# Optimization experiments

Measured on AMD Instinct MI355X. Metric: run time of the kernel, lower is better.

## Reference

```python
import jax, jax.numpy as jnp
from jax import lax
import numpy as np

DN = ('NCHW', 'OIHW', 'NCHW')

def conv2d(x, w, b, pad):
    y = lax.conv_general_dilated(x, w, (1, 1), [(pad, pad), (pad, pad)], dimension_numbers=DN)
    return y + b[None, :, None, None]

def setup_inputs() -> dict:
    key = jax.random.key(0)
    ks = jax.random.split(key, 20)
    B, C, H, W = 2, 256, 64, 64
    d = {}
    d['Fl'] = jax.random.normal(ks[0], (B, C, H, W), dtype=jnp.float32)
    d['Fv'] = jax.random.normal(ks[1], (B, C, H, W), dtype=jnp.float32)
    s3 = 1.0 / np.sqrt(C * 9)
    s1 = 1.0 / np.sqrt(C)
    names3 = ['Wqs', 'Wks', 'Wvs', 'Wqc', 'Wkc', 'Wvc']
    for i, n in enumerate(names3):
        d[n] = jax.random.normal(ks[2 + 2 * i], (C, C, 3, 3), dtype=jnp.float32) * s3
        d['b' + n[1:]] = jax.random.normal(ks[3 + 2 * i], (C,), dtype=jnp.float32) * 0.01
    d['Wgs'] = jax.random.normal(ks[14], (C, C, 1, 1), dtype=jnp.float32) * s1
    d['bgs'] = jax.random.normal(ks[15], (C,), dtype=jnp.float32) * 0.01
    d['Wfuse'] = jax.random.normal(ks[16], (C, 2 * C, 1, 1), dtype=jnp.float32) * (1.0 / np.sqrt(2 * C))
    d['bfuse'] = jax.random.normal(ks[17], (C,), dtype=jnp.float32) * 0.01
    return d

def reference(Fl, Fv, Wqs, bqs, Wks, bks, Wvs, bvs, Wqc, bqc, Wkc, bkc, Wvc, bvc, Wgs, bgs, Wfuse, bfuse):
    b, c, h, w = Fl.shape
    hw = h * w
    # --- self branch (on Fl) ---
    Qs = conv2d(Fl, Wqs, bqs, 1).reshape(b, c, hw)
    Ks = conv2d(Fl, Wks, bks, 1).reshape(b, c, hw)
    Vs = conv2d(Fl, Wvs, bvs, 1).reshape(b, c, hw)
    multi_s = jnp.einsum('bjk,bjq->bkq', Qs, Ks)          # [b, hw, hw]
    multi_s = jax.nn.softmax(multi_s, axis=1)              # softmax over dim=1 (as in torch code)
    Gs = jnp.einsum('bik,bjk->bij', multi_s, Vs)           # [b, hw, c]
    Gs = Gs.reshape(b, c, h, w)                            # raw reshape, faithful to torch
    Gs = conv2d(Gs, Wgs, bgs, 0) + Fl
    # --- cross branch (Q from Fl, K/V from Fv) ---
    Qc = conv2d(Fl, Wqc, bqc, 1).reshape(b, c, hw)
    Kc = conv2d(Fv, Wkc, bkc, 1).reshape(b, c, hw)
    Vc = conv2d(Fv, Wvc, bvc, 1).reshape(b, c, hw)
    multi_c = jnp.einsum('bjk,bjq->bkq', Qc, Kc)
    multi_c = jax.nn.softmax(multi_c, axis=1)
    Gc = jnp.einsum('bik,bjk->bij', multi_c, Vc)
    Gc = Gc.reshape(b, c, h, w)
    Gc = conv2d(Gc, Wgs, bgs, 0) + Fv                      # note: original uses Gs_conv for both branches
    out = conv2d(jnp.concatenate([Gs, Gc], axis=1), Wfuse, bfuse, 0)
    return out
```

## Files before the change

kernel.cpp:

```cpp
#include <hip/hip_runtime.h>

typedef __bf16 bf16x4 __attribute__((ext_vector_type(4)));
typedef __bf16 bf16x8 __attribute__((ext_vector_type(8)));
typedef float  f32x4  __attribute__((ext_vector_type(4)));

#define HWSZ 4096
#define CCH  256
#define LOG2E 1.44269504088896340736f

enum { M_SSTAT = 0, M_CONV = 1, M_G1 = 4, M_FUSE = 5 };

__device__ __forceinline__ float exp2_fast(float x) {
#if __has_builtin(__builtin_amdgcn_exp2f)
  return __builtin_amdgcn_exp2f(x);
#else
  return exp2f(x);
#endif
}

__device__ __forceinline__ void stage16(const __bf16* g, __bf16* ldsBase) {
#if __has_builtin(__builtin_amdgcn_global_load_lds)
  __builtin_amdgcn_global_load_lds(
      (const __attribute__((address_space(1))) void*)g,
      (__attribute__((address_space(3))) void*)ldsBase, 16, 0, 0);
#else
  int lane = threadIdx.x & 63;
  *(bf16x8*)(ldsBase + lane * 8) = *(const bf16x8*)g;
#endif
}

template<int MODE>
__global__ __launch_bounds__(256)
void gemm_bt(const __bf16* __restrict__ A, long sAz,
             const __bf16* __restrict__ B, long sBz,
             int N, int K,
             __bf16* __restrict__ o0, __bf16* __restrict__ o1,
             __bf16* __restrict__ o2, __bf16* __restrict__ o3,
             long sOz,
             float* __restrict__ fout, long sFz,
             const float* __restrict__ bb0, const float* __restrict__ bb1,
             const float* __restrict__ bb2, const float* __restrict__ bb3,
             const float* __restrict__ resid, long sRz,
             float* __restrict__ pmo, float* __restrict__ plo,
             __bf16* __restrict__ o4, __bf16* __restrict__ o5,
             const float* __restrict__ bb4, const float* __restrict__ bb5,
             const __bf16* __restrict__ A2)
{
  __shared__ __align__(16) __bf16 smem[8192];
  __bf16* As = smem;
  __bf16* Bs = smem + 4096;

  const int tid  = threadIdx.x;
  const int lane = tid & 63;
  const int w    = tid >> 6;
  const int wm   = (w >> 1) * 64;
  const int wn   = (w & 1) * 64;
  const int z    = blockIdx.z;
  const int by   = blockIdx.y;
  const int bn   = blockIdx.x * 128;

  int bmEff = by * 128;
  const __bf16* Ab;
  const __bf16* Bb;
  if constexpr (MODE == M_CONV) {
    bool isL = (by < 8);
    bmEff = (isL ? by : by - 8) * 128;
    Ab = isL ? A : A2;
    Bb = B + (long)((isL ? 0 : 2) + z) * sBz;
  } else {
    Ab = A + (long)z * sAz;
    Bb = B + (long)z * sBz;
  }

  f32x4 acc[4][4] = {};

  const int srow = lane >> 2;
  const int skc  = (lane & 3) * 8;

  for (int k0 = 0; k0 < K; k0 += 32) {
#pragma unroll
    for (int j = 0; j < 2; ++j) {
      int rbase = w * 32 + j * 16;
      stage16(Ab + (long)(bmEff + rbase + srow) * K + k0 + skc, As + rbase * 32);
    }
#pragma unroll
    for (int j = 0; j < 2; ++j) {
      int rbase = w * 32 + j * 16;
      stage16(Bb + (long)(bn + rbase + srow) * K + k0 + skc, Bs + rbase * 32);
    }
    __syncthreads();
    bf16x8 af[4], bfr[4];
#pragma unroll
    for (int t = 0; t < 4; ++t)
      af[t] = *(const bf16x8*)(As + (wm + t * 16 + (lane & 15)) * 32 + (lane >> 4) * 8);
#pragma unroll
    for (int t = 0; t < 4; ++t)
      bfr[t] = *(const bf16x8*)(Bs + (wn + t * 16 + (lane & 15)) * 32 + (lane >> 4) * 8);
#pragma unroll
    for (int mt = 0; mt < 4; ++mt)
#pragma unroll
      for (int nt = 0; nt < 4; ++nt)
        acc[mt][nt] = __builtin_amdgcn_mfma_f32_16x16x32_bf16(af[mt], bfr[nt], acc[mt][nt], 0, 0, 0);
    __syncthreads();
  }

  if constexpr (MODE != M_SSTAT) {
#pragma unroll
    for (int mt = 0; mt < 4; ++mt) {
#pragma unroll
      for (int nt = 0; nt < 4; ++nt) {
#pragma unroll
        for (int r = 0; r < 4; ++r) {
          int m = bmEff + wm + mt * 16 + (lane >> 4) * 4 + r;
          int n = bn + wn + nt * 16 + (lane & 15);
          float v = acc[mt][nt][r];
          if constexpr (MODE == M_CONV) {
            int g = m >> 8, mm = m & 255;
            const float* bias; __bf16* op; bool vlay;
            if (by < 8) {
              bias = (g == 0) ? bb0 : (g == 1) ? bb1 : (g == 2) ? bb2 : bb3;
              op   = (g == 0) ? o0  : (g == 1) ? o1  : (g == 2) ? o2  : o3;
              vlay = (g == 2);
            } else {
              bias = g ? bb5 : bb4;
              op   = g ? o5  : o4;
              vlay = (g == 1);
            }
            float vv = v + bias[mm];
            if (vlay) op[(long)z * sOz + (long)mm * HWSZ + n] = (__bf16)vv;
            else      op[(long)z * sOz + (long)n * CCH + mm] = (__bf16)vv;
          } else if constexpr (MODE == M_G1) {
            int bz = z & 1, brr = z >> 1;
            const float* rs = brr ? bb4 : resid;
            float vv = v + bb0[m] + rs[(long)bz * sRz + (long)m * HWSZ + n];
            o0[(long)bz * sOz + (long)n * 512 + m + brr * 256] = (__bf16)vv;
          } else if constexpr (MODE == M_FUSE) {
            fout[(long)z * sFz + (long)m * HWSZ + n] = v + bb0[m];
          }
        }
      }
    }
  }

  if constexpr (MODE == M_SSTAT) {
    __shared__ float sm_[4][64], sl_[4][64];
#pragma unroll
    for (int nt = 0; nt < 4; ++nt) {
      float mx = -3.0e38f;
#pragma unroll
      for (int mt = 0; mt < 4; ++mt)
#pragma unroll
        for (int r = 0; r < 4; ++r) mx = fmaxf(mx, acc[mt][nt][r]);
      float sl = 0.f;
#pragma unroll
      for (int mt = 0; mt < 4; ++mt)
#pragma unroll
        for (int r = 0; r < 4; ++r) sl += exp2_fast((acc[mt][nt][r] - mx) * LOG2E);
#pragma unroll
      for (int d = 16; d <= 32; d <<= 1) {
        float om = __shfl_xor(mx, d, 64);
        float ol = __shfl_xor(sl, d, 64);
        float nm = fmaxf(mx, om);
        sl = sl * exp2_fast((mx - nm) * LOG2E) + ol * exp2_fast((om - nm) * LOG2E);
        mx = nm;
      }
      if (lane < 16) { sm_[w][nt * 16 + lane] = mx; sl_[w][nt * 16 + lane] = sl; }
    }
    __syncthreads();
    if (tid < 128) {
      int hf = tid >> 6, c = tid & 63;
      float m1 = sm_[hf][c],     l1 = sl_[hf][c];
      float m2 = sm_[hf + 2][c], l2 = sl_[hf + 2][c];
      float nm = fmaxf(m1, m2);
      float ll = l1 * exp2_fast((m1 - nm) * LOG2E) + l2 * exp2_fast((m2 - nm) * LOG2E);
      pmo[((long)z * 32 + by) * 4096 + bn + tid] = nm;
      plo[((long)z * 32 + by) * 4096 + bn + tid] = ll;
    }
  }
}

__global__ __launch_bounds__(256)
void fused_pv(const __bf16* __restrict__ qs, const __bf16* __restrict__ qc,
              const __bf16* __restrict__ ks, const __bf16* __restrict__ kc,
              const __bf16* __restrict__ vs, const __bf16* __restrict__ vc,
              const float* __restrict__ mst, const float* __restrict__ lst,
              float* __restrict__ gacc)
{
  __shared__ __align__(16) __bf16 Qres[64 * 260];
  __shared__ __align__(16) __bf16 Pl[64 * 132];
  __shared__ __align__(16) __bf16 Kst[128 * 32];
  __shared__ __align__(16) __bf16 Vst[256 * 32];
  __shared__ float ms_[128], li_[128];

  const int tid = threadIdx.x, lane = tid & 63, w = tid >> 6;
  const int quad = lane >> 4, l15 = lane & 15;
  const int bi  = blockIdx.x * 64;
  const int zbr = blockIdx.y;
  const int qh  = blockIdx.z;
  const int br = zbr >> 1, z = zbr & 1;
  const __bf16* Qt = (br ? qc : qs) + (long)z * 1048576;
  const __bf16* Kt = (br ? kc : ks) + (long)z * 1048576;
  const __bf16* Vv = (br ? vc : vs) + (long)z * 1048576;
  const float* msp = mst + (long)zbr * 4096;
  const float* lsp = lst + (long)zbr * 4096;
  float* go = gacc + ((long)qh * 4 + zbr) * 1048576;

  for (int idx = tid; idx < 2048; idx += 256) {
    int r = idx >> 5, c8 = (idx & 31) * 8;
    *(bf16x8*)(Qres + r * 260 + c8) = *(const bf16x8*)(Qt + (long)(bi + r) * 256 + c8);
  }

  f32x4 accO[4][4] = {};
  const int srow = lane >> 2, skc = (lane & 3) * 8;
  const int q0 = qh * 2048;

  for (int qc0 = q0; qc0 < q0 + 2048; qc0 += 128) {
    if (tid < 128) ms_[tid] = msp[qc0 + tid];
    else           li_[tid - 128] = lsp[qc0 + tid - 128];
    f32x4 accS[4][2] = {};
#pragma unroll
    for (int cs = 0; cs < 256; cs += 32) {
#pragma unroll
      for (int jj = 0; jj < 2; ++jj) {
        int rbase = w * 32 + jj * 16;
        stage16(Kt + (long)(qc0 + rbase + srow) * 256 + cs + skc, Kst + rbase * 32);
      }
      __syncthreads();
      bf16x8 aq[4], bk[2];
#pragma unroll
      for (int mt = 0; mt < 4; ++mt)
        aq[mt] = *(const bf16x8*)(Qres + (mt * 16 + l15) * 260 + cs + quad * 8);
#pragma unroll
      for (int nt = 0; nt < 2; ++nt)
        bk[nt] = *(const bf16x8*)(Kst + (w * 32 + nt * 16 + l15) * 32 + quad * 8);
#pragma unroll
      for (int mt = 0; mt < 4; ++mt)
#pragma unroll
        for (int nt = 0; nt < 2; ++nt)
          accS[mt][nt] = __builtin_amdgcn_mfma_f32_16x16x32_bf16(aq[mt], bk[nt], accS[mt][nt], 0, 0, 0);
      __syncthreads();
    }
#pragma unroll
    for (int mt = 0; mt < 4; ++mt)
#pragma unroll
      for (int nt = 0; nt < 2; ++nt) {
        int q = w * 32 + nt * 16 + l15;
        float mq = ms_[q], lq = li_[q];
#pragma unroll
        for (int r = 0; r < 4; ++r) {
          int i = mt * 16 + quad * 4 + r;
          Pl[i * 132 + q] = (__bf16)(exp2_fast((accS[mt][nt][r] - mq) * LOG2E) * lq);
        }
      }
    __syncthreads();
#pragma unroll
    for (int qs0 = 0; qs0 < 128; qs0 += 32) {
#pragma unroll
      for (int c = 0; c < 4; ++c) {
        int rbase = w * 64 + c * 16;
        stage16(Vv + (long)(rbase + srow) * 4096 + qc0 + qs0 + skc, Vst + rbase * 32);
      }
      __syncthreads();
      bf16x8 ap[4], bv[4];
#pragma unroll
      for (int mt = 0; mt < 4; ++mt)
        ap[mt] = *(const bf16x8*)(Pl + (mt * 16 + l15) * 132 + qs0 + quad * 8);
#pragma unroll
      for (int nt = 0; nt < 4; ++nt)
        bv[nt] = *(const bf16x8*)(Vst + (w * 64 + nt * 16 + l15) * 32 + quad * 8);
#pragma unroll
      for (int mt = 0; mt < 4; ++mt)
#pragma unroll
        for (int nt = 0; nt < 4; ++nt)
          accO[mt][nt] = __builtin_amdgcn_mfma_f32_16x16x32_bf16(ap[mt], bv[nt], accO[mt][nt], 0, 0, 0);
      __syncthreads();
    }
  }
#pragma unroll
  for (int mt = 0; mt < 4; ++mt)
#pragma unroll
    for (int nt = 0; nt < 4; ++nt)
#pragma unroll
      for (int r = 0; r < 4; ++r) {
        int i = mt * 16 + quad * 4 + r;
        int j = w * 64 + nt * 16 + l15;
        go[(long)(bi + i) * 256 + j] = accO[mt][nt][r];
      }
}

__global__ __launch_bounds__(256)
void gsum_reshape(const float* __restrict__ ga, __bf16* __restrict__ gt) {
  __shared__ __bf16 lds[64 * 260];
  const int t = threadIdx.x, lane = t & 63, w = t >> 6;
  const int zbr = blockIdx.z;
  const int v   = blockIdx.y;
  const int jg  = blockIdx.x;
  const float* g0 = ga + (long)zbr * 1048576;
  const float* g1 = g0 + 4194304;
  for (int ci0 = 0; ci0 < 256; ci0 += 4) {
    int ci = ci0 + w;
    long src = (long)(ci * 16 + v) * 256 + jg * 64 + lane;
    lds[lane * 260 + ci] = (__bf16)(g0[src] + g1[src]);
  }
  __syncthreads();
  __bf16* out = gt + (long)zbr * 1048576 + ((long)v * 256 + jg * 64) * 256;
#pragma unroll
  for (int pp = 0; pp < 8; ++pp) {
    int idx = pp * 256 + t;
    int row = idx >> 5, c8 = (idx & 31) * 8;
    *(bf16x8*)(out + (long)row * 256 + c8) = *(const bf16x8*)(lds + row * 260 + c8);
  }
}

__global__ void transpose_cvt(const float* __restrict__ F0, const float* __restrict__ F1,
                              __bf16* __restrict__ Xt) {
  __shared__ float tile[32][33];
  int img = blockIdx.z;
  const float* src = (img < 2 ? F0 : F1) + (long)(img & 1) * (CCH * HWSZ);
  __bf16* dst = Xt + (long)img * (HWSZ * CCH);
  int p0 = blockIdx.x * 32, c0 = blockIdx.y * 32;
  int tx = threadIdx.x, ty = threadIdx.y;
#pragma unroll
  for (int j = 0; j < 32; j += 8)
    tile[ty + j][tx] = src[(long)(c0 + ty + j) * HWSZ + p0 + tx];
  __syncthreads();
#pragma unroll
  for (int j = 0; j < 32; j += 8)
    dst[(long)(p0 + ty + j) * CCH + c0 + tx] = (__bf16)tile[tx][ty + j];
}

__global__ void im2col_k(const __bf16* __restrict__ Xt, __bf16* __restrict__ Cc) {
  int img = blockIdx.y;
  int e = blockIdx.x * 256 + threadIdx.x;
  int p = e / 288;
  int c8 = e - p * 288;
  int t = c8 >> 5;
  int ci0 = (c8 & 31) * 8;
  int dy = t / 3 - 1, dx = t - (t / 3) * 3 - 1;
  int y = p >> 6, x = p & 63;
  int yy = y + dy, xx = x + dx;
  const __bf16* src = Xt + (long)img * (HWSZ * CCH);
  __bf16* dst = Cc + (long)img * 9437184 + (long)p * 2304 + t * 256 + ci0;
  uint4 v = make_uint4(0u, 0u, 0u, 0u);
  if ((unsigned)yy < 64u && (unsigned)xx < 64u)
    v = *(const uint4*)(src + (long)(yy * 64 + xx) * CCH + ci0);
  *(uint4*)dst = v;
}

struct W6 { const float* w[6]; };
__global__ void repack_w3(W6 wp, __bf16* __restrict__ AL, __bf16* __restrict__ AV) {
  int zi = blockIdx.y;
  int e = blockIdx.x * 256 + threadIdx.x;
  int co = e / 2304;
  int rem = e - co * 2304;
  int t = rem >> 8, ci = rem & 255;
  float v = wp.w[zi][(long)co * 2304 + ci * 9 + t];
  __bf16* dst = (zi < 4) ? (AL + (long)zi * 256 * 2304) : (AV + (long)(zi - 4) * 256 * 2304);
  dst[(long)co * 2304 + rem] = (__bf16)v;
}

__global__ void cvt_bf(const float* __restrict__ s, __bf16* __restrict__ d, int n) {
  int i = blockIdx.x * 256 + threadIdx.x;
  if (i < n) d[i] = (__bf16)s[i];
}

__global__ void stats_combine(const float* __restrict__ pm, const float* __restrict__ pl,
                              float* __restrict__ mst, float* __restrict__ lst) {
  int q = blockIdx.x * 256 + threadIdx.x;
  int z = blockIdx.y;
  const float* pmz = pm + (long)z * 32 * 4096;
  const float* plz = pl + (long)z * 32 * 4096;
  float m = -3.0e38f;
#pragma unroll
  for (int rc = 0; rc < 32; ++rc) m = fmaxf(m, pmz[(long)rc * 4096 + q]);
  float l = 0.f;
#pragma unroll
  for (int rc = 0; rc < 32; ++rc)
    l += plz[(long)rc * 4096 + q] * exp2_fast((pmz[(long)rc * 4096 + q] - m) * LOG2E);
  mst[(long)z * 4096 + q] = m;
  lst[(long)z * 4096 + q] = 1.0f / l;
}

extern "C" void kernel_launch(void* const* d_in, const int* in_sizes, int n_in,
                              void* d_out, int out_size, void* d_ws, size_t ws_size,
                              hipStream_t stream) {
  const float* Fl  = (const float*)d_in[0];
  const float* Fv  = (const float*)d_in[1];
  const float* Wqs = (const float*)d_in[2];  const float* bqs = (const float*)d_in[3];
  const float* Wks = (const float*)d_in[4];  const float* bks = (const float*)d_in[5];
  const float* Wvs = (const float*)d_in[6];  const float* bvs = (const float*)d_in[7];
  const float* Wqc = (const float*)d_in[8];  const float* bqc = (const float*)d_in[9];
  const float* Wkc = (const float*)d_in[10]; const float* bkc = (const float*)d_in[11];
  const float* Wvc = (const float*)d_in[12]; const float* bvc = (const float*)d_in[13];
  const float* Wgs = (const float*)d_in[14]; const float* bgs = (const float*)d_in[15];
  const float* Wfu = (const float*)d_in[16]; const float* bfu = (const float*)d_in[17];

  char* ws = (char*)d_ws;
  size_t off = 0;
  auto take = [&](size_t bytes) -> void* {
    void* p = ws + off; off = (off + bytes + 255) & ~(size_t)255; return p;
  };
  __bf16* QST  = (__bf16*)take(4194304);
  __bf16* KST  = (__bf16*)take(4194304);
  __bf16* QCT  = (__bf16*)take(4194304);
  __bf16* KCT  = (__bf16*)take(4194304);
  __bf16* VS   = (__bf16*)take(4194304);
  __bf16* VC   = (__bf16*)take(4194304);
  __bf16* GTS  = (__bf16*)take(8388608);
  __bf16* ZZ   = (__bf16*)take(8388608);
  __bf16* AL   = (__bf16*)take(4718592);
  __bf16* AV   = (__bf16*)take(2359296);
  __bf16* WGSb = (__bf16*)take(131072);
  __bf16* WFSb = (__bf16*)take(262144);
  float*  MST  = (float*)take(65536);
  float*  LST  = (float*)take(65536);
  float*  PM   = (float*)take(1048576);
  float*  PL   = (float*)take(1048576);
  size_t ovl = off;
  __bf16* Xt = (__bf16*)take(8388608);
  __bf16* Cc = (__bf16*)take(75497472);
  size_t needConv = off;
  float* GACC = (float*)(ws + ovl);
  size_t needAttn = ovl + 33554432;
  size_t need = needConv > needAttn ? needConv : needAttn;
  if (ws_size < need) return;

  const long Z1 = 1048576;

  transpose_cvt<<<dim3(128, 8, 4), dim3(32, 8), 0, stream>>>(Fl, Fv, Xt);
  im2col_k<<<dim3(4608, 4), 256, 0, stream>>>(Xt, Cc);
  W6 wp; wp.w[0]=Wqs; wp.w[1]=Wks; wp.w[2]=Wvs; wp.w[3]=Wqc; wp.w[4]=Wkc; wp.w[5]=Wvc;
  repack_w3<<<dim3(2304, 6), 256, 0, stream>>>(wp, AL, AV);
  cvt_bf<<<256, 256, 0, stream>>>(Wgs, WGSb, 65536);
  cvt_bf<<<512, 256, 0, stream>>>(Wfu, WFSb, 131072);

  gemm_bt<M_CONV><<<dim3(32, 12, 2), 256, 0, stream>>>(
      AL, 0, Cc, 9437184, 4096, 2304,
      QST, KST, VS, QCT, Z1,
      nullptr, 0,
      bqs, bks, bvs, bqc,
      nullptr, 0, nullptr, nullptr,
      KCT, VC, bkc, bvc, AV);

  for (int br = 0; br < 2; ++br) {
    const __bf16* Qt = br ? QCT : QST;
    const __bf16* Kt = br ? KCT : KST;
    gemm_bt<M_SSTAT><<<dim3(32, 32, 2), 256, 0, stream>>>(
        Qt, Z1, Kt, Z1, 4096, 256,
        nullptr, nullptr, nullptr, nullptr, 0,
        nullptr, 0,
        nullptr, nullptr, nullptr, nullptr,
        nullptr, 0, PM, PL,
        nullptr, nullptr, nullptr, nullptr, nullptr);
    stats_combine<<<dim3(16, 2), 256, 0, stream>>>(PM, PL, MST + br * 8192, LST + br * 8192);
  }
  fused_pv<<<dim3(64, 4, 2), 256, 0, stream>>>(
      QST, QCT, KST, KCT, VS, VC, MST, LST, GACC);
  gsum_reshape<<<dim3(4, 16, 4), 256, 0, stream>>>(GACC, GTS);

  gemm_bt<M_G1><<<dim3(32, 2, 4), 256, 0, stream>>>(
      WGSb, 0, GTS, Z1, 4096, 256,
      ZZ, nullptr, nullptr, nullptr, (long)2097152,
      nullptr, 0,
      bgs, nullptr, nullptr, nullptr,
      Fl, Z1, nullptr, nullptr,
      nullptr, nullptr, Fv, nullptr, nullptr);
  gemm_bt<M_FUSE><<<dim3(32, 2, 2), 256, 0, stream>>>(
      WFSb, 0, ZZ, (long)2097152, 4096, 512,
      nullptr, nullptr, nullptr, nullptr, 0,
      (float*)d_out, Z1,
      bfu, nullptr, nullptr, nullptr,
      nullptr, 0, nullptr, nullptr,
      nullptr, nullptr, nullptr, nullptr, nullptr);
}
```

Before: 482.7 us.

## Fuse softmax column stats into single streaming kernel; drop LDS staging in fused_pv

The two-pass softmax statistics (a GEMM-tile partial-stats kernel per branch plus a combine kernel) are replaced by one qk_stats kernel. Each block keeps a 64-column K tile in LDS, streams all query rows directly from global memory, and keeps an online max/sum in registers, so the partial-stat buffers and two extra launches per branch go away. fused_pv also stops staging K and V tiles through LDS and loads MFMA operands straight from global memory, which removes many __syncthreads. The cost is uncoalesced, cache-dependent global loads and only 256 blocks of work in qk_stats.

```diff
diff --git a/kernel.cpp b/kernel.cpp
--- a/kernel.cpp
+++ b/kernel.cpp
@@ -8,7 +8,7 @@
 #define CCH  256
 #define LOG2E 1.44269504088896340736f
 
-enum { M_SSTAT = 0, M_CONV = 1, M_G1 = 4, M_FUSE = 5 };
+enum { M_CONV = 1, M_G1 = 4, M_FUSE = 5 };
 
 __device__ __forceinline__ float exp2_fast(float x) {
 #if __has_builtin(__builtin_amdgcn_exp2f)
@@ -41,7 +41,6 @@
              const float* __restrict__ bb0, const float* __restrict__ bb1,
              const float* __restrict__ bb2, const float* __restrict__ bb3,
              const float* __restrict__ resid, long sRz,
-             float* __restrict__ pmo, float* __restrict__ plo,
              __bf16* __restrict__ o4, __bf16* __restrict__ o5,
              const float* __restrict__ bb4, const float* __restrict__ bb5,
              const __bf16* __restrict__ A2)
@@ -104,58 +103,98 @@
     __syncthreads();
   }
 
-  if constexpr (MODE != M_SSTAT) {
-#pragma unroll
-    for (int mt = 0; mt < 4; ++mt) {
-#pragma unroll
-      for (int nt = 0; nt < 4; ++nt) {
-#pragma unroll
-        for (int r = 0; r < 4; ++r) {
-          int m = bmEff + wm + mt * 16 + (lane >> 4) * 4 + r;
-          int n = bn + wn + nt * 16 + (lane & 15);
-          float v = acc[mt][nt][r];
-          if constexpr (MODE == M_CONV) {
-            int g = m >> 8, mm = m & 255;
-            const float* bias; __bf16* op; bool vlay;
-            if (by < 8) {
-              bias = (g == 0) ? bb0 : (g == 1) ? bb1 : (g == 2) ? bb2 : bb3;
-              op   = (g == 0) ? o0  : (g == 1) ? o1  : (g == 2) ? o2  : o3;
-              vlay = (g == 2);
-            } else {
-              bias = g ? bb5 : bb4;
-              op   = g ? o5  : o4;
-              vlay = (g == 1);
-            }
-            float vv = v + bias[mm];
-            if (vlay) op[(long)z * sOz + (long)mm * HWSZ + n] = (__bf16)vv;
-            else      op[(long)z * sOz + (long)n * CCH + mm] = (__bf16)vv;
-          } else if constexpr (MODE == M_G1) {
-            int bz = z & 1, brr = z >> 1;
-            const float* rs = brr ? bb4 : resid;
-            float vv = v + bb0[m] + rs[(long)bz * sRz + (long)m * HWSZ + n];
-            o0[(long)bz * sOz + (long)n * 512 + m + brr * 256] = (__bf16)vv;
-          } else if constexpr (MODE == M_FUSE) {
-            fout[(long)z * sFz + (long)m * HWSZ + n] = v + bb0[m];
+#pragma unroll
+  for (int mt = 0; mt < 4; ++mt) {
+#pragma unroll
+    for (int nt = 0; nt < 4; ++nt) {
+#pragma unroll
+      for (int r = 0; r < 4; ++r) {
+        int m = bmEff + wm + mt * 16 + (lane >> 4) * 4 + r;
+        int n = bn + wn + nt * 16 + (lane & 15);
+        float v = acc[mt][nt][r];
+        if constexpr (MODE == M_CONV) {
+          int g = m >> 8, mm = m & 255;
+          const float* bias; __bf16* op; bool vlay;
+          if (by < 8) {
+            bias = (g == 0) ? bb0 : (g == 1) ? bb1 : (g == 2) ? bb2 : bb3;
+            op   = (g == 0) ? o0  : (g == 1) ? o1  : (g == 2) ? o2  : o3;
+            vlay = (g == 2);
+          } else {
+            bias = g ? bb5 : bb4;
+            op   = g ? o5  : o4;
+            vlay = (g == 1);
           }
+          float vv = v + bias[mm];
+          if (vlay) op[(long)z * sOz + (long)mm * HWSZ + n] = (__bf16)vv;
+          else      op[(long)z * sOz + (long)n * CCH + mm] = (__bf16)vv;
+        } else if constexpr (MODE == M_G1) {
+          int bz = z & 1, brr = z >> 1;
+          const float* rs = brr ? bb4 : resid;
+          float vv = v + bb0[m] + rs[(long)bz * sRz + (long)m * HWSZ + n];
+          o0[(long)bz * sOz + (long)n * 512 + m + brr * 256] = (__bf16)vv;
+        } else if constexpr (MODE == M_FUSE) {
+          fout[(long)z * sFz + (long)m * HWSZ + n] = v + bb0[m];
         }
       }
     }
   }
-
-  if constexpr (MODE == M_SSTAT) {
-    __shared__ float sm_[4][64], sl_[4][64];
+}
+
+__global__ __launch_bounds__(256)
+void qk_stats(const __bf16* __restrict__ qs, const __bf16* __restrict__ qc,
+              const __bf16* __restrict__ ks, const __bf16* __restrict__ kc,
+              float* __restrict__ mst, float* __restrict__ lst)
+{
+  __shared__ __align__(16) __bf16 Kres[64 * 260];
+  __shared__ float wm_[4][64], wl_[4][64];
+
+  const int tid = threadIdx.x, lane = tid & 63, w = tid >> 6;
+  const int quad = lane >> 4, l15 = lane & 15;
+  const int qb = blockIdx.x * 64;
+  const int z = blockIdx.y, br = blockIdx.z;
+  const __bf16* Qt = (br ? qc : qs) + (long)z * 1048576;
+  const __bf16* Kt = (br ? kc : ks) + (long)z * 1048576;
+
+  for (int idx = tid; idx < 2048; idx += 256) {
+    int r = idx >> 5, c8 = (idx & 31) * 8;
+    *(bf16x8*)(Kres + r * 260 + c8) = *(const bf16x8*)(Kt + (long)(qb + r) * 256 + c8);
+  }
+  __syncthreads();
+
+  float rm[4], rl[4];
+#pragma unroll
+  for (int nt = 0; nt < 4; ++nt) { rm[nt] = -3.0e38f; rl[nt] = 0.f; }
+
+  for (int it = 0; it < 16; ++it) {
+    const int i0 = it * 256 + w * 64;
+    f32x4 accS[4][4] = {};
+#pragma unroll
+    for (int cs = 0; cs < 256; cs += 32) {
+      bf16x8 a[4], b[4];
+#pragma unroll
+      for (int mt = 0; mt < 4; ++mt)
+        a[mt] = *(const bf16x8*)(Qt + (long)(i0 + mt * 16 + l15) * 256 + cs + quad * 8);
+#pragma unroll
+      for (int nt = 0; nt < 4; ++nt)
+        b[nt] = *(const bf16x8*)(Kres + (nt * 16 + l15) * 260 + cs + quad * 8);
+#pragma unroll
+      for (int mt = 0; mt < 4; ++mt)
+#pragma unroll
+        for (int nt = 0; nt < 4; ++nt)
+          accS[mt][nt] = __builtin_amdgcn_mfma_f32_16x16x32_bf16(a[mt], b[nt], accS[mt][nt], 0, 0, 0);
+    }
 #pragma unroll
     for (int nt = 0; nt < 4; ++nt) {
       float mx = -3.0e38f;
 #pragma unroll
       for (int mt = 0; mt < 4; ++mt)
 #pragma unroll
-        for (int r = 0; r < 4; ++r) mx = fmaxf(mx, acc[mt][nt][r]);
+        for (int r = 0; r < 4; ++r) mx = fmaxf(mx, accS[mt][nt][r]);
       float sl = 0.f;
 #pragma unroll
       for (int mt = 0; mt < 4; ++mt)
 #pragma unroll
-        for (int r = 0; r < 4; ++r) sl += exp2_fast((acc[mt][nt][r] - mx) * LOG2E);
+        for (int r = 0; r < 4; ++r) sl += exp2_fast((accS[mt][nt][r] - mx) * LOG2E);
 #pragma unroll
       for (int d = 16; d <= 32; d <<= 1) {
         float om = __shfl_xor(mx, d, 64);
@@ -164,18 +203,27 @@
         sl = sl * exp2_fast((mx - nm) * LOG2E) + ol * exp2_fast((om - nm) * LOG2E);
         mx = nm;
       }
-      if (lane < 16) { sm_[w][nt * 16 + lane] = mx; sl_[w][nt * 16 + lane] = sl; }
-    }
-    __syncthreads();
-    if (tid < 128) {
-      int hf = tid >> 6, c = tid & 63;
-      float m1 = sm_[hf][c],     l1 = sl_[hf][c];
-      float m2 = sm_[hf + 2][c], l2 = sl_[hf + 2][c];
-      float nm = fmaxf(m1, m2);
-      float ll = l1 * exp2_fast((m1 - nm) * LOG2E) + l2 * exp2_fast((m2 - nm) * LOG2E);
-      pmo[((long)z * 32 + by) * 4096 + bn + tid] = nm;
-      plo[((long)z * 32 + by) * 4096 + bn + tid] = ll;
-    }
+      float nm = fmaxf(rm[nt], mx);
+      rl[nt] = rl[nt] * exp2_fast((rm[nt] - nm) * LOG2E) + sl * exp2_fast((mx - nm) * LOG2E);
+      rm[nt] = nm;
+    }
+  }
+  if (lane < 16) {
+#pragma unroll
+    for (int nt = 0; nt < 4; ++nt) { wm_[w][nt * 16 + lane] = rm[nt]; wl_[w][nt * 16 + lane] = rl[nt]; }
+  }
+  __syncthreads();
+  if (tid < 64) {
+    float m = -3.0e38f;
+#pragma unroll
+    for (int ww = 0; ww < 4; ++ww) m = fmaxf(m, wm_[ww][tid]);
+    float l = 0.f;
+#pragma unroll
+    for (int ww = 0; ww < 4; ++ww)
+      l += wl_[ww][tid] * exp2_fast((wm_[ww][tid] - m) * LOG2E);
+    long o = ((long)(br * 2 + z)) * 4096 + qb + tid;
+    mst[o] = m;
+    lst[o] = 1.0f / l;
   }
 }
 
@@ -188,8 +236,6 @@
 {
   __shared__ __align__(16) __bf16 Qres[64 * 260];
   __shared__ __align__(16) __bf16 Pl[64 * 132];
-  __shared__ __align__(16) __bf16 Kst[128 * 32];
-  __shared__ __align__(16) __bf16 Vst[256 * 32];
   __shared__ float ms_[128], li_[128];
 
   const int tid = threadIdx.x, lane = tid & 63, w = tid >> 6;
@@ -211,34 +257,27 @@
   }
 
   f32x4 accO[4][4] = {};
-  const int srow = lane >> 2, skc = (lane & 3) * 8;
   const int q0 = qh * 2048;
 
   for (int qc0 = q0; qc0 < q0 + 2048; qc0 += 128) {
     if (tid < 128) ms_[tid] = msp[qc0 + tid];
     else           li_[tid - 128] = lsp[qc0 + tid - 128];
+    __syncthreads();
     f32x4 accS[4][2] = {};
 #pragma unroll
     for (int cs = 0; cs < 256; cs += 32) {
-#pragma unroll
-      for (int jj = 0; jj < 2; ++jj) {
-        int rbase = w * 32 + jj * 16;
-        stage16(Kt + (long)(qc0 + rbase + srow) * 256 + cs + skc, Kst + rbase * 32);
-      }
-      __syncthreads();
       bf16x8 aq[4], bk[2];
 #pragma unroll
       for (int mt = 0; mt < 4; ++mt)
         aq[mt] = *(const bf16x8*)(Qres + (mt * 16 + l15) * 260 + cs + quad * 8);
 #pragma unroll
       for (int nt = 0; nt < 2; ++nt)
-        bk[nt] = *(const bf16x8*)(Kst + (w * 32 + nt * 16 + l15) * 32 + quad * 8);
+        bk[nt] = *(const bf16x8*)(Kt + (long)(qc0 + w * 32 + nt * 16 + l15) * 256 + cs + quad * 8);
 #pragma unroll
       for (int mt = 0; mt < 4; ++mt)
 #pragma unroll
         for (int nt = 0; nt < 2; ++nt)
           accS[mt][nt] = __builtin_amdgcn_mfma_f32_16x16x32_bf16(aq[mt], bk[nt], accS[mt][nt], 0, 0, 0);
-      __syncthreads();
     }
 #pragma unroll
     for (int mt = 0; mt < 4; ++mt)
@@ -255,25 +294,18 @@
     __syncthreads();
 #pragma unroll
     for (int qs0 = 0; qs0 < 128; qs0 += 32) {
-#pragma unroll
-      for (int c = 0; c < 4; ++c) {
-        int rbase = w * 64 + c * 16;
-        stage16(Vv + (long)(rbase + srow) * 4096 + qc0 + qs0 + skc, Vst + rbase * 32);
-      }
-      __syncthreads();
       bf16x8 ap[4], bv[4];
 #pragma unroll
       for (int mt = 0; mt < 4; ++mt)
         ap[mt] = *(const bf16x8*)(Pl + (mt * 16 + l15) * 132 + qs0 + quad * 8);
 #pragma unroll
       for (int nt = 0; nt < 4; ++nt)
-        bv[nt] = *(const bf16x8*)(Vst + (w * 64 + nt * 16 + l15) * 32 + quad * 8);
+        bv[nt] = *(const bf16x8*)(Vv + (long)(w * 64 + nt * 16 + l15) * 4096 + qc0 + qs0 + quad * 8);
 #pragma unroll
       for (int mt = 0; mt < 4; ++mt)
 #pragma unroll
         for (int nt = 0; nt < 4; ++nt)
           accO[mt][nt] = __builtin_amdgcn_mfma_f32_16x16x32_bf16(ap[mt], bv[nt], accO[mt][nt], 0, 0, 0);
-      __syncthreads();
     }
   }
 #pragma unroll
@@ -362,23 +394,6 @@
 __global__ void cvt_bf(const float* __restrict__ s, __bf16* __restrict__ d, int n) {
   int i = blockIdx.x * 256 + threadIdx.x;
   if (i < n) d[i] = (__bf16)s[i];
-}
-
-__global__ void stats_combine(const float* __restrict__ pm, const float* __restrict__ pl,
-                              float* __restrict__ mst, float* __restrict__ lst) {
-  int q = blockIdx.x * 256 + threadIdx.x;
-  int z = blockIdx.y;
-  const float* pmz = pm + (long)z * 32 * 4096;
-  const float* plz = pl + (long)z * 32 * 4096;
-  float m = -3.0e38f;
-#pragma unroll
-  for (int rc = 0; rc < 32; ++rc) m = fmaxf(m, pmz[(long)rc * 4096 + q]);
-  float l = 0.f;
-#pragma unroll
-  for (int rc = 0; rc < 32; ++rc)
-    l += plz[(long)rc * 4096 + q] * exp2_fast((pmz[(long)rc * 4096 + q] - m) * LOG2E);
-  mst[(long)z * 4096 + q] = m;
-  lst[(long)z * 4096 + q] = 1.0f / l;
 }
 
 extern "C" void kernel_launch(void* const* d_in, const int* in_sizes, int n_in,
@@ -414,8 +429,6 @@
   __bf16* WFSb = (__bf16*)take(262144);
   float*  MST  = (float*)take(65536);
   float*  LST  = (float*)take(65536);
-  float*  PM   = (float*)take(1048576);
-  float*  PL   = (float*)take(1048576);
   size_t ovl = off;
   __bf16* Xt = (__bf16*)take(8388608);
   __bf16* Cc = (__bf16*)take(75497472);
@@ -439,21 +452,11 @@
       QST, KST, VS, QCT, Z1,
       nullptr, 0,
       bqs, bks, bvs, bqc,
-      nullptr, 0, nullptr, nullptr,
+      nullptr, 0,
       KCT, VC, bkc, bvc, AV);
 
-  for (int br = 0; br < 2; ++br) {
-    const __bf16* Qt = br ? QCT : QST;
-    const __bf16* Kt = br ? KCT : KST;
-    gemm_bt<M_SSTAT><<<dim3(32, 32, 2), 256, 0, stream>>>(
-        Qt, Z1, Kt, Z1, 4096, 256,
-        nullptr, nullptr, nullptr, nullptr, 0,
-        nullptr, 0,
-        nullptr, nullptr, nullptr, nullptr,
-        nullptr, 0, PM, PL,
-        nullptr, nullptr, nullptr, nullptr, nullptr);
-    stats_combine<<<dim3(16, 2), 256, 0, stream>>>(PM, PL, MST + br * 8192, LST + br * 8192);
-  }
+  qk_stats<<<dim3(64, 2, 2), 256, 0, stream>>>(QST, QCT, KST, KCT, MST, LST);
+
   fused_pv<<<dim3(64, 4, 2), 256, 0, stream>>>(
       QST, QCT, KST, KCT, VS, VC, MST, LST, GACC);
   gsum_reshape<<<dim3(4, 16, 4), 256, 0, stream>>>(GACC, GTS);
@@ -463,13 +466,13 @@
       ZZ, nullptr, nullptr, nullptr, (long)2097152,
       nullptr, 0,
       bgs, nullptr, nullptr, nullptr,
-      Fl, Z1, nullptr, nullptr,
+      Fl, Z1,
       nullptr, nullptr, Fv, nullptr, nullptr);
   gemm_bt<M_FUSE><<<dim3(32, 2, 2), 256, 0, stream>>>(
       WFSb, 0, ZZ, (long)2097152, 4096, 512,
       nullptr, nullptr, nullptr, nullptr, 0,
       (float*)d_out, Z1,
       bfu, nullptr, nullptr, nullptr,
-      nullptr, 0, nullptr, nullptr,
+      nullptr, 0,
       nullptr, nullptr, nullptr, nullptr, nullptr);
 }
```

New measurement: 526.8 us. 1.09x slower.
